# Kernel tuning notes

Hardware: AMD Instinct MI355X
Metric: run time of the kernel (lower is better)

The kernel has to match this reference:

```python
import jax, jax.numpy as jnp
import numpy as np

B, S, H, NH = 2, 2048, 2048, 16
HD = H // NH  # head_dim = 128


def setup_inputs() -> dict:
    key = jax.random.key(0)
    ks = jax.random.split(key, 6)
    scale = 1.0 / np.sqrt(H)
    hidden_state = jax.random.normal(ks[0], (B, S, H), dtype=jnp.float32)
    # upper-triangular (strictly above diagonal) = 1 -> masked positions
    causal_mask = jnp.triu(jnp.ones((S, S), dtype=jnp.float32), k=1)[None, None]
    Wq = jax.random.normal(ks[1], (H, H), dtype=jnp.float32) * scale
    Wk = jax.random.normal(ks[2], (H, H), dtype=jnp.float32) * scale
    Wv = jax.random.normal(ks[3], (H, H), dtype=jnp.float32) * scale
    Wo = jax.random.normal(ks[4], (H, H), dtype=jnp.float32) * scale
    zeros = jnp.zeros((H,), dtype=jnp.float32)
    return {"hidden_state": hidden_state, "causal_mask": causal_mask,
            "Wq": Wq, "bq": zeros, "Wk": Wk, "bk": zeros,
            "Wv": Wv, "bv": zeros, "Wo": Wo, "bo": zeros}


def reference(hidden_state, causal_mask, Wq, bq, Wk, bk, Wv, bv, Wo, bo):
    b, s, h = hidden_state.shape
    q = (hidden_state @ Wq.T + bq).reshape(b, s, NH, HD).transpose(0, 2, 1, 3)  # [B,NH,S,HD]
    k = (hidden_state @ Wk.T + bk).reshape(b, s, NH, HD).transpose(0, 2, 1, 3)
    v = (hidden_state @ Wv.T + bv).reshape(b, s, NH, HD).transpose(0, 2, 1, 3)
    scores = jnp.einsum('bhqd,bhkd->bhqk', q, k) / jnp.sqrt(jnp.float32(HD))
    scores = scores + causal_mask * (-1e9)
    probs = jax.nn.softmax(scores, axis=-1)
    out = jnp.einsum('bhqk,bhkd->bhqd', probs, v)
    out = out.transpose(0, 2, 1, 3).reshape(b, s, h)
    return out @ Wo.T + bo
```

## Files before the change

kernel.cpp:

```cpp
#include <hip/hip_runtime.h>
#include <hip/hip_bf16.h>
#include <stdint.h>

#define B_   2
#define S_   2048
#define H_   2048
#define NH_  16
#define HD_  128
#define MTOT (B_*S_)

typedef __attribute__((ext_vector_type(8))) short bf16x8;
typedef __attribute__((ext_vector_type(4))) short bf16x4;
typedef __attribute__((ext_vector_type(4))) float f32x4;

__device__ __forceinline__ void gload_lds16(const void* g, void* l) {
    __builtin_amdgcn_global_load_lds(
        (const __attribute__((address_space(1))) void*)g,
        (__attribute__((address_space(3))) void*)l, 16, 0, 0);
}

__device__ __forceinline__ unsigned short f2bfu(float x) {
    __hip_bfloat16 h = __float2bfloat16(x);
    return *reinterpret_cast<unsigned short*>(&h);
}
__device__ __forceinline__ int packbf(float a, float b) {
    return (int)f2bfu(a) | ((int)f2bfu(b) << 16);
}

#define BAR()  asm volatile("s_barrier" ::: "memory")
#define WLG0() asm volatile("s_waitcnt lgkmcnt(0)" ::: "memory")
#define WVM(n) asm volatile("s_waitcnt vmcnt(" #n ")" ::: "memory")

__global__ void castk(const float* __restrict__ in, __hip_bfloat16* __restrict__ out, int n4) {
    int i = blockIdx.x * 256 + threadIdx.x;
    if (i < n4) {
        float4 v = *(const float4*)(in + (size_t)i * 4);
        out[(size_t)i*4 + 0] = __float2bfloat16(v.x);
        out[(size_t)i*4 + 1] = __float2bfloat16(v.y);
        out[(size_t)i*4 + 2] = __float2bfloat16(v.z);
        out[(size_t)i*4 + 3] = __float2bfloat16(v.w);
    }
}

__global__ void castw4(const float* __restrict__ w0, const float* __restrict__ w1,
                       const float* __restrict__ w2, const float* __restrict__ w3,
                       __hip_bfloat16* o0, __hip_bfloat16* o1,
                       __hip_bfloat16* o2, __hip_bfloat16* o3, int n4) {
    const float* in; __hip_bfloat16* out;
    switch (blockIdx.y) {
        case 0:  in = w0; out = o0; break;
        case 1:  in = w1; out = o1; break;
        case 2:  in = w2; out = o2; break;
        default: in = w3; out = o3; break;
    }
    int i = blockIdx.x * 256 + threadIdx.x;
    if (i < n4) {
        float4 v = *(const float4*)(in + (size_t)i * 4);
        out[(size_t)i*4 + 0] = __float2bfloat16(v.x);
        out[(size_t)i*4 + 1] = __float2bfloat16(v.y);
        out[(size_t)i*4 + 2] = __float2bfloat16(v.z);
        out[(size_t)i*4 + 3] = __float2bfloat16(v.w);
    }
}

template<int SMEMB, int BF16OUT>
__device__ __forceinline__ void gemm_body(const __hip_bfloat16* __restrict__ Ablk,
                                          const __hip_bfloat16* __restrict__ Wblk,
                                          const float* __restrict__ bias,
                                          void* __restrict__ Cout,
                                          int N, int K, int br, int bc, bool vt)
{
    __shared__ __align__(16) char smem[SMEMB];
    __hip_bfloat16* As = (__hip_bfloat16*)smem;
    __hip_bfloat16* Bs = (__hip_bfloat16*)(smem + 8192);

    const int tid  = threadIdx.x;
    const int wave = tid >> 6, lane = tid & 63;
    const int quad = lane >> 4, l16 = lane & 15;
    const int wr = wave >> 1, wc = wave & 1;

    f32x4 acc[4][4] = {};

    for (int k0 = 0; k0 < K; k0 += 32) {
#pragma unroll
        for (int t = 0; t < 2; ++t) {
            int c = t * 256 + wave * 64 + lane;
            int row = c >> 2, cc = c & 3;
            int base = (t * 256 + wave * 64) * 16;
            gload_lds16(Ablk + (size_t)row * K + k0 + cc * 8, (char*)As + base);
            gload_lds16(Wblk + (size_t)row * K + k0 + cc * 8, (char*)Bs + base);
        }
        __syncthreads();

        bf16x8 af[4], bf[4];
#pragma unroll
        for (int i = 0; i < 4; ++i)
            af[i] = *(const bf16x8*)&As[(wr * 64 + i * 16 + l16) * 32 + quad * 8];
#pragma unroll
        for (int j = 0; j < 4; ++j)
            bf[j] = *(const bf16x8*)&Bs[(wc * 64 + j * 16 + l16) * 32 + quad * 8];

#pragma unroll
        for (int i = 0; i < 4; ++i)
#pragma unroll
            for (int j = 0; j < 4; ++j)
                acc[i][j] = __builtin_amdgcn_mfma_f32_16x16x32_bf16(af[i], bf[j], acc[i][j], 0, 0, 0);
        __syncthreads();
    }

    if (BF16OUT && vt) {
        __hip_bfloat16* Ls = (__hip_bfloat16*)smem;
#pragma unroll
        for (int j = 0; j < 4; ++j) {
            int d = wc * 64 + j * 16 + l16;
            float bv = bias[bc * 128 + d];
#pragma unroll
            for (int i = 0; i < 4; ++i) {
                int t0 = wr * 64 + i * 16 + quad * 4;
#pragma unroll
                for (int r = 0; r < 4; ++r)
                    Ls[d * 136 + t0 + r] = __float2bfloat16(acc[i][j][r] + bv);
            }
        }
        __syncthreads();
        const int bq = br >> 4;
        const int s0 = (br & 15) * 128;
        __hip_bfloat16* VT = (__hip_bfloat16*)Cout;
        const size_t rowbase = (size_t)(bq * 16 + bc) * 128;
#pragma unroll
        for (int rep = 0; rep < 8; ++rep) {
            int L = rep * 256 + tid;
            int d = L >> 4, tch = L & 15;
            bf16x8 v = *(const bf16x8*)&Ls[d * 136 + tch * 8];
            *(bf16x8*)(VT + (rowbase + d) * (size_t)S_ + s0 + tch * 8) = v;
        }
        return;
    }

#pragma unroll
    for (int i = 0; i < 4; ++i) {
        int row = br * 128 + wr * 64 + i * 16 + quad * 4;
#pragma unroll
        for (int j = 0; j < 4; ++j) {
            int col = bc * 128 + wc * 64 + j * 16 + l16;
            float bv = bias[col];
#pragma unroll
            for (int r = 0; r < 4; ++r) {
                float v = acc[i][j][r] + bv;
                if (BF16OUT)
                    ((__hip_bfloat16*)Cout)[(size_t)(row + r) * N + col] = __float2bfloat16(v);
                else
                    ((float*)Cout)[(size_t)(row + r) * N + col] = v;
            }
        }
    }
}

__global__ __launch_bounds__(256)
void gemm_out(const __hip_bfloat16* __restrict__ A, const __hip_bfloat16* __restrict__ W,
              const float* __restrict__ bias, float* __restrict__ C)
{
    gemm_body<16384, 0>(A + (size_t)(blockIdx.y * 128) * H_, W + (size_t)(blockIdx.x * 128) * H_,
                        bias, C, H_, H_, blockIdx.y, blockIdx.x, false);
}

__global__ __launch_bounds__(512, 2)
void gemm_qkv8(const __hip_bfloat16* __restrict__ X,
               const __hip_bfloat16* __restrict__ Wq, const __hip_bfloat16* __restrict__ Wk,
               const __hip_bfloat16* __restrict__ Wv,
               const float* __restrict__ bq, const float* __restrict__ bk,
               const float* __restrict__ bv,
               __hip_bfloat16* __restrict__ Qo, __hip_bfloat16* __restrict__ Ko,
               __hip_bfloat16* __restrict__ VTo)
{
    __shared__ __align__(16) char smem[131072];

    const int bid = blockIdx.x;
    const int swz = (bid & 7) * 48 + (bid >> 3);
    const int sel = swz >> 7;
    const int rem = swz & 127;
    const int bm  = rem & 15;
    const int bn  = rem >> 4;

    const __hip_bfloat16* W = (sel == 0) ? Wq : (sel == 1) ? Wk : Wv;
    const float* bias       = (sel == 0) ? bq : (sel == 1) ? bk : bv;

    const int tid  = threadIdx.x;
    const int wave = tid >> 6, lane = tid & 63;
    const int quad = lane >> 4, l16 = lane & 15;
    const int wr = wave >> 2, wc = wave & 3;

    const int ro = l16 * 64;
    const int co = (((l16 & 8) ? ((quad * 8) ^ 16) : (quad * 8)) << 1);

    int r0, c0, r1, c1;
    {
        int D = tid * 16;
        int rg = D >> 11, cg = (D >> 10) & 1;
        int rr = (D >> 6) & 15, c = (D & 63) >> 1;
        int cs = (rr & 8) ? (c ^ 16) : c;
        r0 = rg * 16 + rr;  c0 = cg * 32 + cs;
        D = 8192 + tid * 16;
        rg = D >> 11; cg = (D >> 10) & 1;
        rr = (D >> 6) & 15; c = (D & 63) >> 1;
        cs = (rr & 8) ? (c ^ 16) : c;
        r1 = rg * 16 + rr;  c1 = cg * 32 + cs;
    }

    const __hip_bfloat16* Xp = X + (size_t)(bm * 256) * H_;
    const __hip_bfloat16* Wp = W + (size_t)(bn * 256) * H_;

    char* const A0h = smem + wr * 16384;
    char* const A1h = smem + 32768 + wr * 16384;
    char* const B0h = smem + 65536 + (wc >> 1) * 16384;
    char* const B1h = smem + 98304 + (wc >> 1) * 16384;
    const int bsub = (wc & 1) * 4;

    auto STG = [&](char* ldsb, const __hip_bfloat16* g) {
        gload_lds16(g + (size_t)r0 * H_ + c0, ldsb + wave * 1024);
        gload_lds16(g + (size_t)r1 * H_ + c1, ldsb + 8192 + wave * 1024);
    };
    auto SRC = [&](const __hip_bfloat16* P, int t, int hf) {
        return P + (size_t)(hf * 128) * H_ + (size_t)t * 64;
    };

    f32x4 acc[8][4] = {};

    STG(smem,                 SRC(Xp, 0, 0));
    STG(smem + 16384,         SRC(Xp, 0, 1));
    STG(smem + 65536,         SRC(Wp, 0, 0));
    STG(smem + 65536 + 16384, SRC(Wp, 0, 1));
    STG(smem + 98304,         SRC(Wp, 1, 0));
    STG(smem + 98304 + 16384, SRC(Wp, 1, 1));
    WVM(4);
    BAR();

    const int NIT = H_ / 128;
    bf16x8 bfr[4][2];
    for (int j = 0; j < NIT; ++j) {
        const bool more = (j < NIT - 1);
        const int t1 = 2 * j + 1;
#pragma unroll
        for (int ph = 0; ph < 8; ++ph) {
            const int p = ph & 3;
            char* aA = (ph < 4) ? A0h : A1h;
            char* aB = (ph < 4) ? B0h : B1h;

            if (p == 0) {
#pragma unroll
                for (int jj = 0; jj < 4; ++jj)
#pragma unroll
                    for (int kk = 0; kk < 2; ++kk)
                        bfr[jj][kk] = *(const bf16x8*)(aB + ((bsub + jj) * 2 + kk) * 1024 + ro + co);
            }
            bf16x8 af[2][2];
#pragma unroll
            for (int i2 = 0; i2 < 2; ++i2)
#pragma unroll
                for (int kk = 0; kk < 2; ++kk)
                    af[i2][kk] = *(const bf16x8*)(aA + ((2 * p + i2) * 2 + kk) * 1024 + ro + co);

            if (ph == 0) { STG(smem + 32768, SRC(Xp, t1, 0));
                           STG(smem + 49152, SRC(Xp, t1, 1)); }
            else if (ph == 1 && more) STG(smem + 65536,          SRC(Wp, t1 + 1, 0));
            else if (ph == 2 && more) STG(smem + 65536 + 16384,  SRC(Wp, t1 + 1, 1));
            else if (ph == 4 && more) STG(smem,                  SRC(Xp, t1 + 1, 0));
            else if (ph == 5 && more) STG(smem + 16384,          SRC(Xp, t1 + 1, 1));
            else if (ph == 6 && more) STG(smem + 98304,          SRC(Wp, t1 + 2, 0));
            else if (ph == 7 && more) STG(smem + 98304 + 16384,  SRC(Wp, t1 + 2, 1));

            if (ph == 3) { if (more) { WVM(4); } else { WVM(0); } }
            if (ph == 7 && more) { WVM(4); }

            BAR();
            WLG0();
            __builtin_amdgcn_sched_barrier(0);
            __builtin_amdgcn_s_setprio(1);
#pragma unroll
            for (int kk = 0; kk < 2; ++kk)
#pragma unroll
                for (int i2 = 0; i2 < 2; ++i2)
#pragma unroll
                    for (int jj = 0; jj < 4; ++jj)
                        acc[2 * p + i2][jj] = __builtin_amdgcn_mfma_f32_16x16x32_bf16(
                            af[i2][kk], bfr[jj][kk], acc[2 * p + i2][jj], 0, 0, 0);
            __builtin_amdgcn_s_setprio(0);
            BAR();
        }
    }

    if (sel < 2) {
        __hip_bfloat16* out = (sel == 0) ? Qo : Ko;
#pragma unroll
        for (int i = 0; i < 8; ++i) {
            int row = bm * 256 + wr * 128 + i * 16 + quad * 4;
#pragma unroll
            for (int jj = 0; jj < 4; ++jj) {
                int col = bn * 256 + wc * 64 + jj * 16 + l16;
                float bv = bias[col];
#pragma unroll
                for (int r = 0; r < 4; ++r)
                    out[(size_t)(row + r) * H_ + col] = __float2bfloat16(acc[i][jj][r] + bv);
            }
        }
    } else {
#pragma unroll
        for (int i = 0; i < 8; ++i) {
            int tok = bm * 256 + wr * 128 + i * 16 + quad * 4;
            int b = tok >> 11, s = tok & (S_ - 1);
#pragma unroll
            for (int jj = 0; jj < 4; ++jj) {
                int col = bn * 256 + wc * 64 + jj * 16 + l16;
                int h = col >> 7, d = col & 127;
                float bv = bias[col];
                bf16x4 v;
#pragma unroll
                for (int r = 0; r < 4; ++r)
                    v[r] = (short)f2bfu(acc[i][jj][r] + bv);
                *(bf16x4*)(VTo + ((size_t)(b * 16 + h) * 128 + d) * S_ + s) = v;
            }
        }
    }
}

__global__ __launch_bounds__(256)
void attn_kernel(const __hip_bfloat16* __restrict__ Q,
                 const __hip_bfloat16* __restrict__ K,
                 const __hip_bfloat16* __restrict__ VT,
                 __hip_bfloat16* __restrict__ O)
{
    __shared__ __align__(16) char Ks[16384];
    __shared__ __align__(16) char Vt[16384];

    const int tid  = threadIdx.x;
    const int wave = tid >> 6, lane = tid & 63;
    const int quad = lane >> 4, l16 = lane & 15;

    const int lid = blockIdx.x;
    const int xcd = lid & 7;
    const int q   = lid >> 3;
    const int bh  = ((q >> 5) << 3) | xcd;
    const int qb  = 31 - (q & 31);
    const int b   = bh >> 4, h = bh & 15;

    const size_t headoff = (size_t)b * S_ * H_ + (size_t)h * HD_;
    const __hip_bfloat16* Qp  = Q + headoff;
    const __hip_bfloat16* Kp  = K + headoff;
    const __hip_bfloat16* Vtp = VT + (size_t)(b * 16 + h) * 128 * S_;

    const float scale = 0.08838834764831843f;
    const int A0 = (((quad & 1) * 2) * 16 + l16) * 4;
    const int A1 = A0 + 64;
    const bool hiq = (quad >= 2);

    const int qrow_local = wave * 16;
    const int qrow = qb * 64 + qrow_local;

    bf16x8 qf[4];
#pragma unroll
    for (int kd = 0; kd < 4; ++kd)
        qf[kd] = *(const bf16x8*)(Qp + (size_t)(qrow + l16) * H_ + kd * 32 + quad * 8);

    f32x4 oacc[8] = {};
    float mi = -1e30f, li = 0.0f;

#pragma unroll
    for (int t = 0; t < 4; ++t) {
        int c = wave * 256 + t * 64 + lane;
        int krow = c >> 4, kpos = c & 15;
        gload_lds16(Kp + (size_t)krow * H_ + (kpos ^ (krow & 7)) * 8,
                    &Ks[(wave * 256 + t * 64) * 16]);
        int vrow = c >> 3, vpos = c & 7;
        gload_lds16(Vtp + (size_t)vrow * S_ + (vpos ^ (vrow & 7)) * 8,
                    &Vt[(wave * 256 + t * 64) * 16]);
    }
    __syncthreads();

    for (int kb = 0; kb <= qb; ++kb) {
        const bool more = (kb < qb);

        f32x4 sacc[4] = {};
        __builtin_amdgcn_s_setprio(1);
#pragma unroll
        for (int cb = 0; cb < 4; ++cb) {
#pragma unroll
            for (int kd = 0; kd < 4; ++kd) {
                int row = cb * 16 + l16;
                int pos = (4 * kd + quad) ^ (l16 & 7);
                bf16x8 kf = *(const bf16x8*)&Ks[row * 256 + pos * 16];
                sacc[cb] = __builtin_amdgcn_mfma_f32_16x16x32_bf16(kf, qf[kd], sacc[cb], 0, 0, 0);
            }
        }
        __builtin_amdgcn_s_setprio(0);

        __syncthreads();

        if (more) {
            const __hip_bfloat16* Kn = Kp + (size_t)(kb + 1) * 64 * H_;
#pragma unroll
            for (int t = 0; t < 4; ++t) {
                int c = wave * 256 + t * 64 + lane;
                int krow = c >> 4, kpos = c & 15;
                gload_lds16(Kn + (size_t)krow * H_ + (kpos ^ (krow & 7)) * 8,
                            &Ks[(wave * 256 + t * 64) * 16]);
            }
        }

        const bool diag = (kb == qb);
        float p[4][4];
        float tm = -1e30f;
#pragma unroll
        for (int cb = 0; cb < 4; ++cb)
#pragma unroll
            for (int r = 0; r < 4; ++r) {
                float s = sacc[cb][r] * scale;
                if (diag) {
                    int keyl = cb * 16 + quad * 4 + r;
                    if (keyl > qrow_local + l16) s = -1e30f;
                }
                p[cb][r] = s;
                tm = fmaxf(tm, s);
            }
        tm = fmaxf(tm, __shfl_xor(tm, 16));
        tm = fmaxf(tm, __shfl_xor(tm, 32));
        float mnew = fmaxf(mi, tm);
        float sum = 0.0f;
#pragma unroll
        for (int cb = 0; cb < 4; ++cb)
#pragma unroll
            for (int r = 0; r < 4; ++r) {
                float e = __expf(p[cb][r] - mnew);
                p[cb][r] = e;
                sum += e;
            }
        sum += __shfl_xor(sum, 16);
        sum += __shfl_xor(sum, 32);
        float alpha = __expf(mi - mnew);
        li = li * alpha + sum;
        mi = mnew;

        float ar[4];
#pragma unroll
        for (int r = 0; r < 4; ++r)
            ar[r] = __shfl(alpha, quad * 4 + r);
#pragma unroll
        for (int db = 0; db < 8; ++db)
#pragma unroll
            for (int r = 0; r < 4; ++r)
                oacc[db][r] *= ar[r];

        int Pp[4][2];
#pragma unroll
        for (int cb = 0; cb < 4; ++cb) {
            Pp[cb][0] = packbf(p[cb][0], p[cb][1]);
            Pp[cb][1] = packbf(p[cb][2], p[cb][3]);
        }
        bf16x8 pf[2];
#pragma unroll
        for (int ks = 0; ks < 2; ++ks) {
            int c0 = 2 * ks, c1 = 2 * ks + 1;
            int d0 = __builtin_amdgcn_ds_bpermute(A0, Pp[c0][0]);
            int e0 = __builtin_amdgcn_ds_bpermute(A0, Pp[c1][0]);
            int d1 = __builtin_amdgcn_ds_bpermute(A0, Pp[c0][1]);
            int e1 = __builtin_amdgcn_ds_bpermute(A0, Pp[c1][1]);
            int d2 = __builtin_amdgcn_ds_bpermute(A1, Pp[c0][0]);
            int e2 = __builtin_amdgcn_ds_bpermute(A1, Pp[c1][0]);
            int d3 = __builtin_amdgcn_ds_bpermute(A1, Pp[c0][1]);
            int e3 = __builtin_amdgcn_ds_bpermute(A1, Pp[c1][1]);
            union { int i[4]; bf16x8 v; } u;
            u.i[0] = hiq ? e0 : d0;
            u.i[1] = hiq ? e1 : d1;
            u.i[2] = hiq ? e2 : d2;
            u.i[3] = hiq ? e3 : d3;
            pf[ks] = u.v;
        }

        __builtin_amdgcn_s_setprio(1);
#pragma unroll
        for (int ks = 0; ks < 2; ++ks) {
#pragma unroll
            for (int db = 0; db < 8; ++db) {
                int vrow = db * 16 + l16;
                int vpos = (ks * 4 + quad) ^ (l16 & 7);
                bf16x8 vf = *(const bf16x8*)&Vt[vrow * 128 + vpos * 16];
                oacc[db] = __builtin_amdgcn_mfma_f32_16x16x32_bf16(pf[ks], vf, oacc[db], 0, 0, 0);
            }
        }
        __builtin_amdgcn_s_setprio(0);

        __syncthreads();

        if (more) {
            const int vcol = (kb + 1) * 64;
#pragma unroll
            for (int t = 0; t < 4; ++t) {
                int c = wave * 256 + t * 64 + lane;
                int vrow = c >> 3, vpos = c & 7;
                gload_lds16(Vtp + (size_t)vrow * S_ + vcol + (vpos ^ (vrow & 7)) * 8,
                            &Vt[(wave * 256 + t * 64) * 16]);
            }
        }
    }

    float lr[4];
#pragma unroll
    for (int r = 0; r < 4; ++r)
        lr[r] = __shfl(li, quad * 4 + r);
#pragma unroll
    for (int db = 0; db < 8; ++db)
#pragma unroll
        for (int r = 0; r < 4; ++r) {
            float v = oacc[db][r] / lr[r];
            size_t row = (size_t)b * S_ + qrow + quad * 4 + r;
            O[row * H_ + h * HD_ + db * 16 + l16] = __float2bfloat16(v);
        }
}

extern "C" void kernel_launch(void* const* d_in, const int* in_sizes, int n_in,
                              void* d_out, int out_size, void* d_ws, size_t ws_size,
                              hipStream_t stream)
{
    const float* hs = (const float*)d_in[0];
    const float* Wq = (const float*)d_in[2];
    const float* bq = (const float*)d_in[3];
    const float* Wk = (const float*)d_in[4];
    const float* bk = (const float*)d_in[5];
    const float* Wv = (const float*)d_in[6];
    const float* bv = (const float*)d_in[7];
    const float* Wo = (const float*)d_in[8];
    const float* bo = (const float*)d_in[9];

    const size_t szX = (size_t)MTOT * H_;
    const size_t szW = (size_t)H_ * H_;

    __hip_bfloat16* Xbf = (__hip_bfloat16*)d_ws;
    __hip_bfloat16* Wqb = Xbf + szX;
    __hip_bfloat16* Wkb = Wqb + szW;
    __hip_bfloat16* Wvb = Wkb + szW;
    __hip_bfloat16* Wob = Wvb + szW;
    __hip_bfloat16* Qb  = Wob + szW;
    __hip_bfloat16* Kb  = Qb + szX;
    __hip_bfloat16* VTb = Kb + szX;

    castk<<<(int)((szX/4 + 255)/256), 256, 0, stream>>>(hs, Xbf, (int)(szX/4));
    dim3 wgrid((unsigned)((szW/4 + 255)/256), 4);
    castw4<<<wgrid, 256, 0, stream>>>(Wq, Wk, Wv, Wo, Wqb, Wkb, Wvb, Wob, (int)(szW/4));

    gemm_qkv8<<<dim3(384), 512, 0, stream>>>(Xbf, Wqb, Wkb, Wvb, bq, bk, bv, Qb, Kb, VTb);

    attn_kernel<<<dim3(1024), 256, 0, stream>>>(Qb, Kb, VTb, Xbf);

    gemm_out<<<dim3(16, 32), 256, 0, stream>>>(Xbf, Wob, bo, (float*)d_out);
}
```

Before: 421.8 us.

## Reuse 256x256 pipelined GEMM body for output projection and drop attention setprio

Moves the 256x256-tile, 512-thread, double-buffered GEMM core from the QKV kernel into a shared templated body with three epilogues: bf16, transposed V, and fp32. The output projection now uses this body with an XCD-aware block mapping instead of the simple 128x128 single-buffered GEMM. This should improve data reuse and latency hiding for the final projection. It also removes the s_setprio hints around the MFMA loops in the attention kernel. The projection now launches only 128 blocks, which may underfill the GPU's CUs.

```diff
diff --git a/kernel.cpp b/kernel.cpp
--- a/kernel.cpp
+++ b/kernel.cpp
@@ -63,128 +63,13 @@
     }
 }
 
-template<int SMEMB, int BF16OUT>
-__device__ __forceinline__ void gemm_body(const __hip_bfloat16* __restrict__ Ablk,
-                                          const __hip_bfloat16* __restrict__ Wblk,
-                                          const float* __restrict__ bias,
-                                          void* __restrict__ Cout,
-                                          int N, int K, int br, int bc, bool vt)
+template<int EPI>
+__device__ __forceinline__ void gemm256_body(const __hip_bfloat16* __restrict__ Xp,
+                                             const __hip_bfloat16* __restrict__ Wp,
+                                             const float* __restrict__ bias,
+                                             void* __restrict__ Cout,
+                                             int bm, int bn, char* smem)
 {
-    __shared__ __align__(16) char smem[SMEMB];
-    __hip_bfloat16* As = (__hip_bfloat16*)smem;
-    __hip_bfloat16* Bs = (__hip_bfloat16*)(smem + 8192);
-
-    const int tid  = threadIdx.x;
-    const int wave = tid >> 6, lane = tid & 63;
-    const int quad = lane >> 4, l16 = lane & 15;
-    const int wr = wave >> 1, wc = wave & 1;
-
-    f32x4 acc[4][4] = {};
-
-    for (int k0 = 0; k0 < K; k0 += 32) {
-#pragma unroll
-        for (int t = 0; t < 2; ++t) {
-            int c = t * 256 + wave * 64 + lane;
-            int row = c >> 2, cc = c & 3;
-            int base = (t * 256 + wave * 64) * 16;
-            gload_lds16(Ablk + (size_t)row * K + k0 + cc * 8, (char*)As + base);
-            gload_lds16(Wblk + (size_t)row * K + k0 + cc * 8, (char*)Bs + base);
-        }
-        __syncthreads();
-
-        bf16x8 af[4], bf[4];
-#pragma unroll
-        for (int i = 0; i < 4; ++i)
-            af[i] = *(const bf16x8*)&As[(wr * 64 + i * 16 + l16) * 32 + quad * 8];
-#pragma unroll
-        for (int j = 0; j < 4; ++j)
-            bf[j] = *(const bf16x8*)&Bs[(wc * 64 + j * 16 + l16) * 32 + quad * 8];
-
-#pragma unroll
-        for (int i = 0; i < 4; ++i)
-#pragma unroll
-            for (int j = 0; j < 4; ++j)
-                acc[i][j] = __builtin_amdgcn_mfma_f32_16x16x32_bf16(af[i], bf[j], acc[i][j], 0, 0, 0);
-        __syncthreads();
-    }
-
-    if (BF16OUT && vt) {
-        __hip_bfloat16* Ls = (__hip_bfloat16*)smem;
-#pragma unroll
-        for (int j = 0; j < 4; ++j) {
-            int d = wc * 64 + j * 16 + l16;
-            float bv = bias[bc * 128 + d];
-#pragma unroll
-            for (int i = 0; i < 4; ++i) {
-                int t0 = wr * 64 + i * 16 + quad * 4;
-#pragma unroll
-                for (int r = 0; r < 4; ++r)
-                    Ls[d * 136 + t0 + r] = __float2bfloat16(acc[i][j][r] + bv);
-            }
-        }
-        __syncthreads();
-        const int bq = br >> 4;
-        const int s0 = (br & 15) * 128;
-        __hip_bfloat16* VT = (__hip_bfloat16*)Cout;
-        const size_t rowbase = (size_t)(bq * 16 + bc) * 128;
-#pragma unroll
-        for (int rep = 0; rep < 8; ++rep) {
-            int L = rep * 256 + tid;
-            int d = L >> 4, tch = L & 15;
-            bf16x8 v = *(const bf16x8*)&Ls[d * 136 + tch * 8];
-            *(bf16x8*)(VT + (rowbase + d) * (size_t)S_ + s0 + tch * 8) = v;
-        }
-        return;
-    }
-
-#pragma unroll
-    for (int i = 0; i < 4; ++i) {
-        int row = br * 128 + wr * 64 + i * 16 + quad * 4;
-#pragma unroll
-        for (int j = 0; j < 4; ++j) {
-            int col = bc * 128 + wc * 64 + j * 16 + l16;
-            float bv = bias[col];
-#pragma unroll
-            for (int r = 0; r < 4; ++r) {
-                float v = acc[i][j][r] + bv;
-                if (BF16OUT)
-                    ((__hip_bfloat16*)Cout)[(size_t)(row + r) * N + col] = __float2bfloat16(v);
-                else
-                    ((float*)Cout)[(size_t)(row + r) * N + col] = v;
-            }
-        }
-    }
-}
-
-__global__ __launch_bounds__(256)
-void gemm_out(const __hip_bfloat16* __restrict__ A, const __hip_bfloat16* __restrict__ W,
-              const float* __restrict__ bias, float* __restrict__ C)
-{
-    gemm_body<16384, 0>(A + (size_t)(blockIdx.y * 128) * H_, W + (size_t)(blockIdx.x * 128) * H_,
-                        bias, C, H_, H_, blockIdx.y, blockIdx.x, false);
-}
-
-__global__ __launch_bounds__(512, 2)
-void gemm_qkv8(const __hip_bfloat16* __restrict__ X,
-               const __hip_bfloat16* __restrict__ Wq, const __hip_bfloat16* __restrict__ Wk,
-               const __hip_bfloat16* __restrict__ Wv,
-               const float* __restrict__ bq, const float* __restrict__ bk,
-               const float* __restrict__ bv,
-               __hip_bfloat16* __restrict__ Qo, __hip_bfloat16* __restrict__ Ko,
-               __hip_bfloat16* __restrict__ VTo)
-{
-    __shared__ __align__(16) char smem[131072];
-
-    const int bid = blockIdx.x;
-    const int swz = (bid & 7) * 48 + (bid >> 3);
-    const int sel = swz >> 7;
-    const int rem = swz & 127;
-    const int bm  = rem & 15;
-    const int bn  = rem >> 4;
-
-    const __hip_bfloat16* W = (sel == 0) ? Wq : (sel == 1) ? Wk : Wv;
-    const float* bias       = (sel == 0) ? bq : (sel == 1) ? bk : bv;
-
     const int tid  = threadIdx.x;
     const int wave = tid >> 6, lane = tid & 63;
     const int quad = lane >> 4, l16 = lane & 15;
@@ -207,9 +92,6 @@
         r1 = rg * 16 + rr;  c1 = cg * 32 + cs;
     }
 
-    const __hip_bfloat16* Xp = X + (size_t)(bm * 256) * H_;
-    const __hip_bfloat16* Wp = W + (size_t)(bn * 256) * H_;
-
     char* const A0h = smem + wr * 16384;
     char* const A1h = smem + 32768 + wr * 16384;
     char* const B0h = smem + 65536 + (wc >> 1) * 16384;
@@ -289,21 +171,8 @@
         }
     }
 
-    if (sel < 2) {
-        __hip_bfloat16* out = (sel == 0) ? Qo : Ko;
-#pragma unroll
-        for (int i = 0; i < 8; ++i) {
-            int row = bm * 256 + wr * 128 + i * 16 + quad * 4;
-#pragma unroll
-            for (int jj = 0; jj < 4; ++jj) {
-                int col = bn * 256 + wc * 64 + jj * 16 + l16;
-                float bv = bias[col];
-#pragma unroll
-                for (int r = 0; r < 4; ++r)
-                    out[(size_t)(row + r) * H_ + col] = __float2bfloat16(acc[i][jj][r] + bv);
-            }
-        }
-    } else {
+    if (EPI == 2) {
+        __hip_bfloat16* VTo = (__hip_bfloat16*)Cout;
 #pragma unroll
         for (int i = 0; i < 8; ++i) {
             int tok = bm * 256 + wr * 128 + i * 16 + quad * 4;
@@ -320,7 +189,68 @@
                 *(bf16x4*)(VTo + ((size_t)(b * 16 + h) * 128 + d) * S_ + s) = v;
             }
         }
-    }
+    } else {
+#pragma unroll
+        for (int i = 0; i < 8; ++i) {
+            int row = bm * 256 + wr * 128 + i * 16 + quad * 4;
+#pragma unroll
+            for (int jj = 0; jj < 4; ++jj) {
+                int col = bn * 256 + wc * 64 + jj * 16 + l16;
+                float bv = bias[col];
+#pragma unroll
+                for (int r = 0; r < 4; ++r) {
+                    float v = acc[i][jj][r] + bv;
+                    if (EPI == 1)
+                        ((__hip_bfloat16*)Cout)[(size_t)(row + r) * H_ + col] = __float2bfloat16(v);
+                    else
+                        ((float*)Cout)[(size_t)(row + r) * H_ + col] = v;
+                }
+            }
+        }
+    }
+}
+
+__global__ __launch_bounds__(512, 2)
+void gemm_qkv8(const __hip_bfloat16* __restrict__ X,
+               const __hip_bfloat16* __restrict__ Wq, const __hip_bfloat16* __restrict__ Wk,
+               const __hip_bfloat16* __restrict__ Wv,
+               const float* __restrict__ bq, const float* __restrict__ bk,
+               const float* __restrict__ bv,
+               __hip_bfloat16* __restrict__ Qo, __hip_bfloat16* __restrict__ Ko,
+               __hip_bfloat16* __restrict__ VTo)
+{
+    __shared__ __align__(16) char smem[131072];
+
+    const int bid = blockIdx.x;
+    const int swz = (bid & 7) * 48 + (bid >> 3);
+    const int sel = swz >> 7;
+    const int rem = swz & 127;
+    const int bm  = rem & 15;
+    const int bn  = rem >> 4;
+
+    const __hip_bfloat16* W = (sel == 0) ? Wq : (sel == 1) ? Wk : Wv;
+    const float* bias       = (sel == 0) ? bq : (sel == 1) ? bk : bv;
+
+    const __hip_bfloat16* Xp = X + (size_t)(bm * 256) * H_;
+    const __hip_bfloat16* Wp = W + (size_t)(bn * 256) * H_;
+
+    if (sel == 2)
+        gemm256_body<2>(Xp, Wp, bias, VTo, bm, bn, smem);
+    else
+        gemm256_body<1>(Xp, Wp, bias, (sel == 0) ? Qo : Ko, bm, bn, smem);
+}
+
+__global__ __launch_bounds__(512, 2)
+void gemm_out8(const __hip_bfloat16* __restrict__ A, const __hip_bfloat16* __restrict__ W,
+               const float* __restrict__ bias, float* __restrict__ C)
+{
+    __shared__ __align__(16) char smem[131072];
+    const int bid = blockIdx.x;
+    const int xcd = bid & 7, i = bid >> 3;
+    const int bm  = (xcd & 3) * 4 + (i & 3);
+    const int bn  = (xcd >> 2) * 4 + (i >> 2);
+    gemm256_body<0>(A + (size_t)(bm * 256) * H_, W + (size_t)(bn * 256) * H_,
+                    bias, C, bm, bn, smem);
 }
 
 __global__ __launch_bounds__(256)
@@ -380,7 +310,6 @@
         const bool more = (kb < qb);
 
         f32x4 sacc[4] = {};
-        __builtin_amdgcn_s_setprio(1);
 #pragma unroll
         for (int cb = 0; cb < 4; ++cb) {
 #pragma unroll
@@ -391,7 +320,6 @@
                 sacc[cb] = __builtin_amdgcn_mfma_f32_16x16x32_bf16(kf, qf[kd], sacc[cb], 0, 0, 0);
             }
         }
-        __builtin_amdgcn_s_setprio(0);
 
         __syncthreads();
 
@@ -475,7 +403,6 @@
             pf[ks] = u.v;
         }
 
-        __builtin_amdgcn_s_setprio(1);
 #pragma unroll
         for (int ks = 0; ks < 2; ++ks) {
 #pragma unroll
@@ -486,7 +413,6 @@
                 oacc[db] = __builtin_amdgcn_mfma_f32_16x16x32_bf16(pf[ks], vf, oacc[db], 0, 0, 0);
             }
         }
-        __builtin_amdgcn_s_setprio(0);
 
         __syncthreads();
 
@@ -550,5 +476,5 @@
 
     attn_kernel<<<dim3(1024), 256, 0, stream>>>(Qb, Kb, VTb, Xbf);
 
-    gemm_out<<<dim3(16, 32), 256, 0, stream>>>(Xbf, Wob, bo, (float*)d_out);
-}
+    gemm_out8<<<dim3(128), 512, 0, stream>>>(Xbf, Wob, bo, (float*)d_out);
+}
```

After: 419.6 us. About the same (-0.5%).
